# Performance work log

Measured on AMD Instinct MI355X. Metric: run time of the kernel, lower is better.

Reference implementation:

```python
import jax, jax.numpy as jnp
import numpy as np

NEG_INF = -1e9

def setup_inputs() -> dict:
    key = jax.random.key(0)
    k1, k2, k3, k4, k5 = jax.random.split(key, 5)
    B, Lq, Lk, D = 8, 2048, 2048, 256
    query = jax.random.normal(k1, (B, Lq, D), dtype=jnp.float32)
    key_t = jax.random.normal(k2, (B, Lk, D), dtype=jnp.float32)
    value = jax.random.normal(k3, (B, Lk, D), dtype=jnp.float32)
    mask = jax.random.randint(k4, (B, Lq, Lk), 0, 2, dtype=jnp.int32)
    # nn.Linear(d_k, 1, bias=False) weight, flattened to [d_k]
    w_align = jax.random.normal(k5, (D,), dtype=jnp.float32) / jnp.sqrt(jnp.float32(D))
    return {"query": query, "key": key_t, "value": value, "mask": mask, "w_align": w_align}

def reference(query, key, value, mask, w_align):
    # Bahdanau additive scores: w . (q_i + k_j). Since the alignment layer is
    # linear, distribute it: score[b,i,j] = (q[b,i] . w) + (k[b,j] . w),
    # avoiding the [B,Lq,Lk,D] broadcast intermediate (same math exactly).
    sq = jnp.einsum('bqd,d->bq', query, w_align)   # [B,Lq]
    sk = jnp.einsum('bkd,d->bk', key, w_align)     # [B,Lk]
    scores = sq[:, :, None] + sk[:, None, :]       # [B,Lq,Lk]
    scores = jnp.where(mask == 0, NEG_INF, scores)
    p_attn = jax.nn.softmax(scores, axis=-1)
    return jnp.matmul(p_attn, value)               # [B,Lq,Dv]
```

## Files before the change

### kernel.cpp

```cpp
#include <hip/hip_runtime.h>
#include <hip/hip_bf16.h>


#define NB 8
#define LQ 2048
#define LK 2048
#define DD 256

typedef __attribute__((ext_vector_type(8))) short short8v;
typedef __attribute__((ext_vector_type(8))) unsigned short ushort8v;
typedef __attribute__((ext_vector_type(4))) float f32x4;

__device__ inline unsigned short f2bf(float x) {
  union { __hip_bfloat16 h; unsigned short u; } cv;
  cv.h = __float2bfloat16(x);
  return cv.u;
}

__device__ inline uint2 pack_mask4(const int4 a) {
  uint2 p;
  p.x = (a.x ? 0x3F80u : 0u) | (a.y ? 0x3F800000u : 0u);
  p.y = (a.z ? 0x3F80u : 0u) | (a.w ? 0x3F800000u : 0u);
  return p;
}

__global__ __launch_bounds__(256) void bah_precompute(
    const float* __restrict__ key, const float* __restrict__ value,
    const float* __restrict__ w, unsigned short* __restrict__ evB,
    unsigned short* __restrict__ eb)
{
  __shared__ float e_s[32];
  __shared__ unsigned short t_s[32][260];

  const int t = threadIdx.x;
  const int lane = t & 63;
  const int wid = t >> 6;
  const int blk = blockIdx.x;
  const int b = blk & 7;
  const int ks = blk >> 3;
  const int j0 = ks * 32;

  const float4 wv4 = reinterpret_cast<const float4*>(w)[lane];

#pragma unroll
  for (int r8 = 0; r8 < 8; ++r8) {
    const int r = wid * 8 + r8;
    const size_t row = (size_t)b * LK + j0 + r;
    const float4 kv = reinterpret_cast<const float4*>(key + row * DD)[lane];
    float s = kv.x * wv4.x + kv.y * wv4.y + kv.z * wv4.z + kv.w * wv4.w;
#pragma unroll
    for (int off = 32; off; off >>= 1) s += __shfl_xor(s, off);
    const float e = __expf(s);
    if (lane == 0) { e_s[r] = e; eb[row] = f2bf(e); }
  }
  __syncthreads();

#pragma unroll
  for (int g = 0; g < 8; ++g) {
    const int jr = g * 4 + wid;
    const size_t row = (size_t)b * LK + j0 + jr;
    const float4 vv = reinterpret_cast<const float4*>(value + row * DD)[lane];
    const float e = e_s[jr];
    ushort4 u;
    u.x = f2bf(e * vv.x);
    u.y = f2bf(e * vv.y);
    u.z = f2bf(e * vv.z);
    u.w = f2bf(e * vv.w);
    *reinterpret_cast<ushort4*>(&t_s[jr][lane * 4]) = u;
  }
  __syncthreads();

  const int lr = lane & 15;
  const int lj = lane >> 4;
#pragma unroll
  for (int n4 = 0; n4 < 4; ++n4) {
    const int n = wid * 4 + n4;
    ushort8v va;
#pragma unroll
    for (int i = 0; i < 8; ++i) va[i] = t_s[lj * 8 + i][n * 16 + lr];
    *reinterpret_cast<ushort8v*>(
        evB + ((size_t)((b * 64 + ks) * 16 + n) * 64 + lane) * 8) = va;
  }
}

__global__ __launch_bounds__(512, 1) void bah_gemm(
    const int* __restrict__ mask, const unsigned short* __restrict__ evB,
    const unsigned short* __restrict__ eb, float* __restrict__ out)
{
  __shared__ unsigned short A_s[3][64 * 64];
  __shared__ float denom_s[64];

  const int t = threadIdx.x;
  const int lane = t & 63;
  const int wid = t >> 6;
  const int wm = wid >> 2;
  const int wn = wid & 3;
  const int lr = lane & 15;
  const int lj = lane >> 4;

  const int blk = blockIdx.x;
  const int b = blk & 7;
  const int i0 = (blk >> 3) * 64;

  const int sr = t >> 3;
  const int q = t & 7;
  const int* aptr = mask + ((size_t)b * LQ + i0 + sr) * LK + q * 4;
  int awr[2];
#pragma unroll
  for (int j = 0; j < 2; ++j)
    awr[j] = sr * 64 + ((((q >> 1) + j * 4 + sr) & 7) * 8) + (q & 1) * 4;

  const unsigned short* bB[4];
#pragma unroll
  for (int nn = 0; nn < 4; ++nn)
    bB[nn] = evB + ((size_t)(b * 64) * 16 + wn * 4 + nn) * 512 + lane * 8;
  const unsigned short* ebb = eb + b * LK + lj * 8;

  int afo[2][2];
#pragma unroll
  for (int m = 0; m < 2; ++m) {
    const int row = wm * 32 + m * 16 + lr;
#pragma unroll
    for (int h = 0; h < 2; ++h)
      afo[m][h] = row * 64 + (((h * 4 + lj + row) & 7) * 8);
  }

  f32x4 acc[2][4] = {};
  f32x4 accd[2] = {};
  const short8v z8 = {};

  short8v bfr[2][2][4];
  short8v efr[2][2] = {{z8, z8}, {z8, z8}};

#pragma unroll
  for (int j = 0; j < 2; ++j) {
    const int4 p = *reinterpret_cast<const int4*>(aptr + j * 32);
    *reinterpret_cast<uint2*>(&A_s[0][awr[j]]) = pack_mask4(p);
  }
  int4 aC0 = *reinterpret_cast<const int4*>(aptr + 64);
  int4 aC1 = *reinterpret_cast<const int4*>(aptr + 64 + 32);
#pragma unroll
  for (int h = 0; h < 2; ++h) {
#pragma unroll
    for (int nn = 0; nn < 4; ++nn)
      bfr[0][h][nn] = *reinterpret_cast<const short8v*>(bB[nn] + (size_t)h * 8192);
    if (wn == 0 && lr == 0)
      efr[0][h] = *reinterpret_cast<const short8v*>(ebb + h * 32);
  }
  __syncthreads();

#pragma unroll 2
  for (int tt = 0; tt < 32; ++tt) {
    const int cur = tt & 1;
    const int nxt = cur ^ 1;
    const int bufC = tt % 3;
    const int bufW = (tt + 1) % 3;

    const int k2 = ((tt + 2) & 31) * 64;
    const int4 aN0 = *reinterpret_cast<const int4*>(aptr + k2);
    const int4 aN1 = *reinterpret_cast<const int4*>(aptr + k2 + 32);
    const int kn = ((tt + 1) & 31) * 2;
#pragma unroll
    for (int h = 0; h < 2; ++h) {
#pragma unroll
      for (int nn = 0; nn < 4; ++nn)
        bfr[nxt][h][nn] = *reinterpret_cast<const short8v*>(
            bB[nn] + (size_t)(kn + h) * 8192);
      short8v ev = z8;
      if (wn == 0 && lr == 0)
        ev = *reinterpret_cast<const short8v*>(ebb + (kn + h) * 32);
      efr[nxt][h] = ev;
    }
    __builtin_amdgcn_sched_barrier(0);

    *reinterpret_cast<uint2*>(&A_s[bufW][awr[0]]) = pack_mask4(aC0);
    *reinterpret_cast<uint2*>(&A_s[bufW][awr[1]]) = pack_mask4(aC1);
    asm volatile("s_waitcnt lgkmcnt(0)" ::: "memory");
    __builtin_amdgcn_sched_barrier(0);
    __builtin_amdgcn_s_barrier();
    __builtin_amdgcn_sched_barrier(0);

#pragma unroll
    for (int h = 0; h < 2; ++h) {
      short8v af[2];
#pragma unroll
      for (int m = 0; m < 2; ++m)
        af[m] = *reinterpret_cast<const short8v*>(&A_s[bufC][afo[m][h]]);
      __builtin_amdgcn_s_setprio(1);
      if (wn == 0) {
#pragma unroll
        for (int m = 0; m < 2; ++m)
          accd[m] = __builtin_amdgcn_mfma_f32_16x16x32_bf16(
              af[m], efr[cur][h], accd[m], 0, 0, 0);
      }
#pragma unroll
      for (int m = 0; m < 2; ++m)
#pragma unroll
        for (int nn = 0; nn < 4; ++nn)
          acc[m][nn] = __builtin_amdgcn_mfma_f32_16x16x32_bf16(
              af[m], bfr[cur][h][nn], acc[m][nn], 0, 0, 0);
      __builtin_amdgcn_s_setprio(0);
    }
    aC0 = aN0; aC1 = aN1;
  }

  if (wn == 0 && lr == 0) {
#pragma unroll
    for (int m = 0; m < 2; ++m)
#pragma unroll
      for (int qq = 0; qq < 4; ++qq)
        denom_s[wm * 32 + m * 16 + lj * 4 + qq] = accd[m][qq];
  }
  __syncthreads();

#pragma unroll
  for (int m = 0; m < 2; ++m) {
    const int row0 = wm * 32 + m * 16 + lj * 4;
    float inv[4];
#pragma unroll
    for (int qq = 0; qq < 4; ++qq) {
      const float dn = denom_s[row0 + qq];
      inv[qq] = (dn != 0.f) ? 1.f / dn : 0.f;
    }
#pragma unroll
    for (int nn = 0; nn < 4; ++nn) {
      const int col = wn * 64 + nn * 16 + lr;
#pragma unroll
      for (int qq = 0; qq < 4; ++qq)
        out[((size_t)b * LQ + (i0 + row0 + qq)) * DD + col] = acc[m][nn][qq] * inv[qq];
    }
  }
}

extern "C" void kernel_launch(void* const* d_in, const int* in_sizes, int n_in,
                              void* d_out, int out_size, void* d_ws, size_t ws_size,
                              hipStream_t stream) {
  const float* key   = (const float*)d_in[1];
  const float* value = (const float*)d_in[2];
  const int*   mask  = (const int*)d_in[3];
  const float* w     = (const float*)d_in[4];
  float* out = (float*)d_out;

  unsigned short* evB = (unsigned short*)d_ws;
  unsigned short* eb  = (unsigned short*)((char*)d_ws + (size_t)NB * DD * LK * 2);

  bah_precompute<<<NB * (LK / 32), 256, 0, stream>>>(key, value, w, evB, eb);
  bah_gemm<<<256, 512, 0, stream>>>(mask, evB, eb, out);
}
```

Baseline: 51.13 us.

## Fuse precompute into GEMM kernel with cooperative launch and per-tile flags

Merges the key/value precompute kernel into the masked GEMM kernel. Each block builds the two 32-row evB slices matching its own q-tile index and publishes a release flag. Consumers then walk the K dimension in a rotated order starting at their own slice, spin-waiting on the flag of each other slice. This removes a kernel launch boundary and lets the precompute overlap with mask loading and the GEMM. In exchange it adds a memset, a cooperative launch, spin-wait polling, more shared memory, and a mask load path that uses only half the threads with wider per-thread loads.

After: 94.27 us. +84.4%, slower.

```diff
diff --git a/kernel.cpp b/kernel.cpp
--- a/kernel.cpp
+++ b/kernel.cpp
@@ -24,92 +24,99 @@
   return p;
 }
 
-__global__ __launch_bounds__(256) void bah_precompute(
+__global__ __launch_bounds__(512, 1) void bah_fused(
     const float* __restrict__ key, const float* __restrict__ value,
-    const float* __restrict__ w, unsigned short* __restrict__ evB,
-    unsigned short* __restrict__ eb)
+    const float* __restrict__ w, const int* __restrict__ mask,
+    unsigned short* __restrict__ evB, unsigned short* __restrict__ eb,
+    unsigned int* __restrict__ flags, float* __restrict__ out)
 {
-  __shared__ float e_s[32];
-  __shared__ unsigned short t_s[32][260];
+  __shared__ unsigned short A_s[3][64 * 64];
+  __shared__ unsigned short pre_s[2][32][260];
+  __shared__ float e_s[2][32];
+  __shared__ float denom_s[64];
 
   const int t = threadIdx.x;
   const int lane = t & 63;
-  const int wid = t >> 6;
   const int blk = blockIdx.x;
   const int b = blk & 7;
-  const int ks = blk >> 3;
-  const int j0 = ks * 32;
-
-  const float4 wv4 = reinterpret_cast<const float4*>(w)[lane];
-
-#pragma unroll
-  for (int r8 = 0; r8 < 8; ++r8) {
-    const int r = wid * 8 + r8;
-    const size_t row = (size_t)b * LK + j0 + r;
-    const float4 kv = reinterpret_cast<const float4*>(key + row * DD)[lane];
-    float s = kv.x * wv4.x + kv.y * wv4.y + kv.z * wv4.z + kv.w * wv4.w;
-#pragma unroll
-    for (int off = 32; off; off >>= 1) s += __shfl_xor(s, off);
-    const float e = __expf(s);
-    if (lane == 0) { e_s[r] = e; eb[row] = f2bf(e); }
-  }
-  __syncthreads();
-
-#pragma unroll
-  for (int g = 0; g < 8; ++g) {
-    const int jr = g * 4 + wid;
-    const size_t row = (size_t)b * LK + j0 + jr;
-    const float4 vv = reinterpret_cast<const float4*>(value + row * DD)[lane];
-    const float e = e_s[jr];
-    ushort4 u;
-    u.x = f2bf(e * vv.x);
-    u.y = f2bf(e * vv.y);
-    u.z = f2bf(e * vv.z);
-    u.w = f2bf(e * vv.w);
-    *reinterpret_cast<ushort4*>(&t_s[jr][lane * 4]) = u;
-  }
-  __syncthreads();
-
-  const int lr = lane & 15;
-  const int lj = lane >> 4;
-#pragma unroll
-  for (int n4 = 0; n4 < 4; ++n4) {
-    const int n = wid * 4 + n4;
-    ushort8v va;
-#pragma unroll
-    for (int i = 0; i < 8; ++i) va[i] = t_s[lj * 8 + i][n * 16 + lr];
-    *reinterpret_cast<ushort8v*>(
-        evB + ((size_t)((b * 64 + ks) * 16 + n) * 64 + lane) * 8) = va;
-  }
-}
-
-__global__ __launch_bounds__(512, 1) void bah_gemm(
-    const int* __restrict__ mask, const unsigned short* __restrict__ evB,
-    const unsigned short* __restrict__ eb, float* __restrict__ out)
-{
-  __shared__ unsigned short A_s[3][64 * 64];
-  __shared__ float denom_s[64];
-
-  const int t = threadIdx.x;
-  const int lane = t & 63;
+  const int itile = blk >> 3;
+  const int i0 = itile * 64;
+
+  const int sr = (t & 255) >> 2;
+  const int q = t & 3;
+  const int* amask = mask + ((size_t)b * LQ + i0 + sr) * LK + q * 4;
+  int awr[4];
+#pragma unroll
+  for (int j = 0; j < 4; ++j)
+    awr[j] = sr * 64 + ((((q >> 1) + 2 * j + sr) & 7) * 8) + (q & 1) * 4;
+
+  int4 aP[4], aC[4];
+  if (t < 256) {
+#pragma unroll
+    for (int j = 0; j < 4; ++j)
+      aP[j] = *reinterpret_cast<const int4*>(amask + itile * 64 + j * 16);
+    const int s1 = (itile + 1) & 31;
+#pragma unroll
+    for (int j = 0; j < 4; ++j)
+      aC[j] = *reinterpret_cast<const int4*>(amask + s1 * 64 + j * 16);
+  }
+
+  {
+    const int hh = t >> 8;
+    const int tq = t & 255;
+    const int wid4 = tq >> 6;
+    const int ks = 2 * itile + hh;
+    const int j0 = ks * 32;
+    const float4 wv4 = reinterpret_cast<const float4*>(w)[lane];
+#pragma unroll
+    for (int r8 = 0; r8 < 8; ++r8) {
+      const int r = wid4 * 8 + r8;
+      const size_t row = (size_t)b * LK + j0 + r;
+      const float4 kv = reinterpret_cast<const float4*>(key + row * DD)[lane];
+      float s = kv.x * wv4.x + kv.y * wv4.y + kv.z * wv4.z + kv.w * wv4.w;
+#pragma unroll
+      for (int off = 32; off; off >>= 1) s += __shfl_xor(s, off);
+      const float e = __expf(s);
+      if (lane == 0) { e_s[hh][r] = e; eb[row] = f2bf(e); }
+    }
+    __syncthreads();
+#pragma unroll
+    for (int g = 0; g < 8; ++g) {
+      const int jr = g * 4 + wid4;
+      const size_t row = (size_t)b * LK + j0 + jr;
+      const float4 vv = reinterpret_cast<const float4*>(value + row * DD)[lane];
+      const float e = e_s[hh][jr];
+      ushort4 u;
+      u.x = f2bf(e * vv.x);
+      u.y = f2bf(e * vv.y);
+      u.z = f2bf(e * vv.z);
+      u.w = f2bf(e * vv.w);
+      *reinterpret_cast<ushort4*>(&pre_s[hh][jr][lane * 4]) = u;
+    }
+    __syncthreads();
+    const int lr_ = lane & 15;
+    const int lj_ = lane >> 4;
+#pragma unroll
+    for (int n4 = 0; n4 < 4; ++n4) {
+      const int n = wid4 * 4 + n4;
+      ushort8v va;
+#pragma unroll
+      for (int i = 0; i < 8; ++i) va[i] = pre_s[hh][lj_ * 8 + i][n * 16 + lr_];
+      *reinterpret_cast<ushort8v*>(
+          evB + (size_t)((b * 64 + ks) * 16 + n) * 512 + (size_t)lane * 8) = va;
+    }
+    __syncthreads();
+    if (t == 0)
+      __hip_atomic_store(&flags[b * 32 + itile], 1u, __ATOMIC_RELEASE,
+                         __HIP_MEMORY_SCOPE_AGENT);
+  }
+
   const int wid = t >> 6;
   const int wm = wid >> 2;
   const int wn = wid & 3;
   const int lr = lane & 15;
   const int lj = lane >> 4;
 
-  const int blk = blockIdx.x;
-  const int b = blk & 7;
-  const int i0 = (blk >> 3) * 64;
-
-  const int sr = t >> 3;
-  const int q = t & 7;
-  const int* aptr = mask + ((size_t)b * LQ + i0 + sr) * LK + q * 4;
-  int awr[2];
-#pragma unroll
-  for (int j = 0; j < 2; ++j)
-    awr[j] = sr * 64 + ((((q >> 1) + j * 4 + sr) & 7) * 8) + (q & 1) * 4;
-
   const unsigned short* bB[4];
 #pragma unroll
   for (int nn = 0; nn < 4; ++nn)
@@ -128,24 +135,22 @@
   f32x4 acc[2][4] = {};
   f32x4 accd[2] = {};
   const short8v z8 = {};
-
   short8v bfr[2][2][4];
   short8v efr[2][2] = {{z8, z8}, {z8, z8}};
 
-#pragma unroll
-  for (int j = 0; j < 2; ++j) {
-    const int4 p = *reinterpret_cast<const int4*>(aptr + j * 32);
-    *reinterpret_cast<uint2*>(&A_s[0][awr[j]]) = pack_mask4(p);
-  }
-  int4 aC0 = *reinterpret_cast<const int4*>(aptr + 64);
-  int4 aC1 = *reinterpret_cast<const int4*>(aptr + 64 + 32);
+  if (t < 256) {
+#pragma unroll
+    for (int j = 0; j < 4; ++j)
+      *reinterpret_cast<uint2*>(&A_s[0][awr[j]]) = pack_mask4(aP[j]);
+  }
 #pragma unroll
   for (int h = 0; h < 2; ++h) {
 #pragma unroll
     for (int nn = 0; nn < 4; ++nn)
-      bfr[0][h][nn] = *reinterpret_cast<const short8v*>(bB[nn] + (size_t)h * 8192);
+      bfr[0][h][nn] = *reinterpret_cast<const short8v*>(
+          bB[nn] + (size_t)(2 * itile + h) * 8192);
     if (wn == 0 && lr == 0)
-      efr[0][h] = *reinterpret_cast<const short8v*>(ebb + h * 32);
+      efr[0][h] = *reinterpret_cast<const short8v*>(ebb + (2 * itile + h) * 32);
   }
   __syncthreads();
 
@@ -155,26 +160,44 @@
     const int nxt = cur ^ 1;
     const int bufC = tt % 3;
     const int bufW = (tt + 1) % 3;
-
-    const int k2 = ((tt + 2) & 31) * 64;
-    const int4 aN0 = *reinterpret_cast<const int4*>(aptr + k2);
-    const int4 aN1 = *reinterpret_cast<const int4*>(aptr + k2 + 32);
-    const int kn = ((tt + 1) & 31) * 2;
+    const int sW = (itile + tt + 2) & 31;
+    const int sB = (itile + tt + 1) & 31;
+
+    int4 aN[4];
+    if (t < 256) {
+#pragma unroll
+      for (int j = 0; j < 4; ++j)
+        aN[j] = *reinterpret_cast<const int4*>(amask + sW * 64 + j * 16);
+    }
+    if (sB != itile) {
+      unsigned int f;
+      do {
+        f = 1u;
+        if (lane == 0)
+          f = __hip_atomic_load(&flags[b * 32 + sB], __ATOMIC_RELAXED,
+                                __HIP_MEMORY_SCOPE_AGENT);
+        f = (unsigned int)__shfl((int)f, 0);
+        if (f == 0u) __builtin_amdgcn_s_sleep(2);
+      } while (f == 0u);
+    }
 #pragma unroll
     for (int h = 0; h < 2; ++h) {
 #pragma unroll
       for (int nn = 0; nn < 4; ++nn)
         bfr[nxt][h][nn] = *reinterpret_cast<const short8v*>(
-            bB[nn] + (size_t)(kn + h) * 8192);
+            bB[nn] + (size_t)(2 * sB + h) * 8192);
       short8v ev = z8;
       if (wn == 0 && lr == 0)
-        ev = *reinterpret_cast<const short8v*>(ebb + (kn + h) * 32);
+        ev = *reinterpret_cast<const short8v*>(ebb + (2 * sB + h) * 32);
       efr[nxt][h] = ev;
     }
     __builtin_amdgcn_sched_barrier(0);
 
-    *reinterpret_cast<uint2*>(&A_s[bufW][awr[0]]) = pack_mask4(aC0);
-    *reinterpret_cast<uint2*>(&A_s[bufW][awr[1]]) = pack_mask4(aC1);
+    if (t < 256) {
+#pragma unroll
+      for (int j = 0; j < 4; ++j)
+        *reinterpret_cast<uint2*>(&A_s[bufW][awr[j]]) = pack_mask4(aC[j]);
+    }
     asm volatile("s_waitcnt lgkmcnt(0)" ::: "memory");
     __builtin_amdgcn_sched_barrier(0);
     __builtin_amdgcn_s_barrier();
@@ -201,7 +224,8 @@
               af[m], bfr[cur][h][nn], acc[m][nn], 0, 0, 0);
       __builtin_amdgcn_s_setprio(0);
     }
-    aC0 = aN0; aC1 = aN1;
+#pragma unroll
+    for (int j = 0; j < 4; ++j) aC[j] = aN[j];
   }
 
   if (wn == 0 && lr == 0) {
@@ -243,7 +267,12 @@
 
   unsigned short* evB = (unsigned short*)d_ws;
   unsigned short* eb  = (unsigned short*)((char*)d_ws + (size_t)NB * DD * LK * 2);
-
-  bah_precompute<<<NB * (LK / 32), 256, 0, stream>>>(key, value, w, evB, eb);
-  bah_gemm<<<256, 512, 0, stream>>>(mask, evB, eb, out);
-}
+  unsigned int* flags = (unsigned int*)((char*)d_ws + (size_t)NB * DD * LK * 2
+                                        + (size_t)NB * LK * 2);
+
+  hipMemsetAsync(flags, 0, NB * 32 * sizeof(unsigned int), stream);
+  void* args[] = {(void*)&key, (void*)&value, (void*)&w, (void*)&mask,
+                  (void*)&evB, (void*)&eb, (void*)&flags, (void*)&out};
+  hipLaunchCooperativeKernel((void*)bah_fused, dim3(256), dim3(512),
+                             args, 0, stream);
+}
```
